# Kernel tuning notes

Measured on AMD Instinct MI355X. Metric: run time of the kernel, lower is better.

## Reference

```python
import jax, jax.numpy as jnp
import numpy as np

DIM = 1024
HEADS = 16
DIM_HEAD = 64
INNER = HEADS * DIM_HEAD
SCALE = DIM_HEAD ** -0.5


def setup_inputs() -> dict:
    key = jax.random.key(0)
    k1, k2, k3 = jax.random.split(key, 3)
    b, n = 2, 2048
    x = jax.random.normal(k1, (b, n, DIM), dtype=jnp.float32)
    mask = jnp.ones((b, n), dtype=bool)
    # to_qkv: Linear(dim, 3*inner, bias=False) stored as [dim, 3*inner]
    w_qkv = jax.random.normal(k2, (DIM, 3 * INNER), dtype=jnp.float32) * (DIM ** -0.5)
    # to_out: Linear(inner, dim, bias=False) stored as [inner, dim]
    w_out = jax.random.normal(k3, (INNER, DIM), dtype=jnp.float32) * (INNER ** -0.5)
    g = jnp.ones((DIM,), dtype=jnp.float32)  # LayerNorm gain
    return {"x": x, "mask": mask, "w_qkv": w_qkv, "w_out": w_out, "g": g}


def _layernorm(x, g):
    eps = 1e-5 if x.dtype == jnp.float32 else 1e-3
    mean = jnp.mean(x, axis=-1, keepdims=True)
    var = jnp.var(x, axis=-1, keepdims=True)  # unbiased=False
    return (x - mean) * jax.lax.rsqrt(var + eps) * g


def reference(x, mask, w_qkv, w_out, g):
    b, n, _ = x.shape
    qkv = x @ w_qkv  # [b, n, 3*inner]
    q, k, v = jnp.split(qkv, 3, axis=-1)
    # b n (h d) -> b h n d
    split_heads = lambda t: t.reshape(b, n, HEADS, DIM_HEAD).transpose(0, 2, 1, 3)
    q, k, v = split_heads(q), split_heads(k), split_heads(v)
    q = q * SCALE
    sim = jnp.einsum('bhid,bhjd->bhij', q, k)  # [b, h, n, n]
    mask_value = -jnp.finfo(sim.dtype).max
    key_mask = mask[:, None, None, :]  # b 1 1 j
    sim = jnp.where(key_mask, sim, mask_value)
    causal_mask = jnp.triu(jnp.ones((n, n), dtype=bool), k=1)
    sim = jnp.where(causal_mask, mask_value, sim)
    attn = jax.nn.softmax(sim.astype(jnp.float32), axis=-1).astype(sim.dtype)
    out = jnp.einsum('bhij,bhjd->bhid', attn, v)
    out = out.transpose(0, 2, 1, 3).reshape(b, n, INNER)  # b h n d -> b n (h d)
    out = out @ w_out
    return _layernorm(out, g)
```

## Files before the change

### kernel.cpp

```cpp
#include <hip/hip_runtime.h>
#include <hip/hip_bf16.h>


typedef __bf16 bf16_t;
typedef __bf16 bf16x8 __attribute__((ext_vector_type(8)));
typedef __bf16 bf16x4 __attribute__((ext_vector_type(4)));
typedef float  f32x4  __attribute__((ext_vector_type(4)));
typedef short  s16x4  __attribute__((ext_vector_type(4)));

#define DIMX   1024
#define HEADS  16
#define DHEAD  64
#define INNER  1024
#define SEQ    2048
#define BATCH  2
#define NROWS  (BATCH * SEQ)
#define QKV_N  (3 * INNER)
#define NQT    (SEQ / 64)
#define QK2SCALE 0.18033688011f

__device__ __forceinline__ bf16_t f2b(float f) { return (bf16_t)f; }

__device__ __forceinline__ void gload16(const bf16_t* g, bf16_t* s) {
  __builtin_amdgcn_global_load_lds(
      (const __attribute__((address_space(1))) unsigned int*)g,
      (__attribute__((address_space(3))) unsigned int*)s, 16, 0, 0);
}

__device__ __forceinline__ f32x4 mfma16(bf16x8 a, bf16x8 b, f32x4 c) {
  return __builtin_amdgcn_mfma_f32_16x16x32_bf16(a, b, c, 0, 0, 0);
}

__device__ __forceinline__ f32x4 pv_mfma(bf16x4 a, bf16x4 b, f32x4 c) {
  s16x4 as, bs;
  __builtin_memcpy(&as, &a, 8);
  __builtin_memcpy(&bs, &b, 8);
#if __has_builtin(__builtin_amdgcn_mfma_f32_16x16x16bf16_1k)
  return __builtin_amdgcn_mfma_f32_16x16x16bf16_1k(as, bs, c, 0, 0, 0);
#else
  f32x4 d = c;
  asm("v_mfma_f32_16x16x16_bf16 %0, %1, %2, %0" : "+v"(d) : "v"(as), "v"(bs));
  return d;
#endif
}

__global__ __launch_bounds__(256)
void prep_all(const float* __restrict__ x, const float* __restrict__ w_qkv,
              const float* __restrict__ w_out, bf16_t* __restrict__ xb,
              bf16_t* __restrict__ wqkvT, bf16_t* __restrict__ woutT) {
  __shared__ float tile[32][33];
  const int bid = blockIdx.x;
  if (bid < 4096) {
    const int i = bid * 256 + threadIdx.x;
    float4 v = *(const float4*)&x[(size_t)i * 4];
    bf16x4 o;
    o[0] = f2b(v.x); o[1] = f2b(v.y); o[2] = f2b(v.z); o[3] = f2b(v.w);
    *(bf16x4*)&xb[(size_t)i * 4] = o;
    return;
  }
  const float* in; bf16_t* out; int R, C, bx, by;
  if (bid < 4096 + 3072) {
    const int t1 = bid - 4096;
    in = w_qkv; out = wqkvT; R = DIMX; C = QKV_N; bx = t1 % 96; by = t1 / 96;
  } else {
    const int t2 = bid - 7168;
    in = w_out; out = woutT; R = DIMX; C = DIMX; bx = t2 & 31; by = t2 >> 5;
  }
  const int c0 = bx * 32, r0 = by * 32;
  const int tx = threadIdx.x & 31, ty = threadIdx.x >> 5;
  #pragma unroll
  for (int i = 0; i < 32; i += 8)
    tile[ty + i][tx] = in[(size_t)(r0 + ty + i) * C + c0 + tx];
  __syncthreads();
  #pragma unroll
  for (int i = 0; i < 32; i += 8)
    out[(size_t)(c0 + ty + i) * R + r0 + tx] = f2b(tile[tx][ty + i]);
}

__global__ __launch_bounds__(256)
void vtrans(const bf16_t* __restrict__ qkv, bf16_t* __restrict__ vt) {
  __shared__ bf16_t t[64][66];
  const int bh = blockIdx.y;
  const int b = bh >> 4, h = bh & 15;
  const int j0 = blockIdx.x * 64;
  const int tx = threadIdx.x & 63, ty = threadIdx.x >> 6;
  #pragma unroll
  for (int i = 0; i < 64; i += 4)
    t[ty + i][tx] = qkv[(size_t)(b * SEQ + j0 + ty + i) * QKV_N + 2 * INNER + h * 64 + tx];
  __syncthreads();
  #pragma unroll
  for (int i = 0; i < 64; i += 4)
    vt[((size_t)bh * 64 + ty + i) * SEQ + j0 + tx] = t[tx][ty + i];
}

template<int OUT_F32>
__global__ __launch_bounds__(256)
void gemm_bt(const bf16_t* __restrict__ A, const bf16_t* __restrict__ Bt,
             void* __restrict__ Cp, int M, int N, int K) {
  constexpr int BK = 64;
  __shared__ bf16_t As[128 * BK];
  __shared__ bf16_t Bs[128 * BK];
  const int t = threadIdx.x;
  const int w = t >> 6, l = t & 63, lo = l & 15, hi = l >> 4;
  const int nwg = gridDim.x * gridDim.y;
  int flat = blockIdx.y * gridDim.x + blockIdx.x;
  if ((nwg & 7) == 0) flat = (flat & 7) * (nwg >> 3) + (flat >> 3);
  const int m0 = (flat / gridDim.x) * 128, n0 = (flat % gridDim.x) * 128;
  const int wm = (w >> 1) * 64, wn = (w & 1) * 64;
  const int sl  = l >> 3;
  const int sgc = ((l & 7) ^ sl) * 8;
  const int r7  = lo & 7;
  f32x4 acc[4][4] = {};
  for (int k0 = 0; k0 < K; k0 += BK) {
    #pragma unroll
    for (int c = 0; c < 4; ++c) {
      const int rb = w * 32 + c * 8;
      gload16(&A [(size_t)(m0 + rb + sl) * K + k0 + sgc], &As[rb * BK + l * 8]);
      gload16(&Bt[(size_t)(n0 + rb + sl) * K + k0 + sgc], &Bs[rb * BK + l * 8]);
    }
    __syncthreads();
    #pragma unroll
    for (int kk = 0; kk < 2; ++kk) {
      bf16x8 af[4], bfr[4];
      #pragma unroll
      for (int mi = 0; mi < 4; ++mi)
        af[mi] = *(const bf16x8*)&As[(wm + mi * 16 + lo) * BK +
                                     (((kk * 4 + hi) ^ r7) << 3)];
      #pragma unroll
      for (int nj = 0; nj < 4; ++nj)
        bfr[nj] = *(const bf16x8*)&Bs[(wn + nj * 16 + lo) * BK +
                                      (((kk * 4 + hi) ^ r7) << 3)];
      __builtin_amdgcn_s_setprio(1);
      #pragma unroll
      for (int mi = 0; mi < 4; ++mi)
        #pragma unroll
        for (int nj = 0; nj < 4; ++nj)
          acc[mi][nj] = mfma16(af[mi], bfr[nj], acc[mi][nj]);
      __builtin_amdgcn_s_setprio(0);
    }
    __syncthreads();
  }
  #pragma unroll
  for (int mi = 0; mi < 4; ++mi)
    #pragma unroll
    for (int nj = 0; nj < 4; ++nj)
      #pragma unroll
      for (int r = 0; r < 4; ++r) {
        size_t row = m0 + wm + mi * 16 + hi * 4 + r;
        size_t col = n0 + wn + nj * 16 + lo;
        if (OUT_F32)
          ((float*)Cp)[row * N + col] = acc[mi][nj][r];
        else
          ((bf16_t*)Cp)[row * N + col] = f2b(acc[mi][nj][r]);
      }
}

__global__ __launch_bounds__(256, 4)
void attn_fa10(const bf16_t* __restrict__ qkv, const bf16_t* __restrict__ vt,
               bf16_t* __restrict__ attn_out, bf16_t* __restrict__ pacc,
               float* __restrict__ plsum) {
  const int bx  = blockIdx.x;
  const int xcd = bx & 7, idx = bx >> 3;
  const int bh  = xcd * 4 + (idx & 3);
  const int ta  = (idx >> 2) & 15;
  const int half = idx >> 6;
  const int tb  = NQT - 1 - ta;
  const int b = bh >> 4, h = bh & 15;
  const int t = threadIdx.x, w = t >> 6, l = t & 63, lo = l & 15, hi = l >> 4;

  __shared__ bf16_t Ks[2][64 * 64];
  __shared__ bf16_t Vs[2][64 * 64];

  const int srow = l >> 3;
  const int sgc  = ((l & 7) ^ srow) * 8;
  const size_t kgbase = (size_t)(b * SEQ) * QKV_N + INNER + h * 64;
  const size_t vgbase = (size_t)bh * 64 * SEQ;

  auto STAGE = [&](int ti, int buf) {
    const int j0 = ti * 64;
    #pragma unroll
    for (int c = 0; c < 2; ++c) {
      const int rb = w * 16 + c * 8;
      gload16(&qkv[kgbase + (size_t)(j0 + rb + srow) * QKV_N + sgc],
              &Ks[buf][rb * 64]);
      gload16(&vt[vgbase + (size_t)(rb + srow) * SEQ + j0 + sgc],
              &Vs[buf][rb * 64]);
    }
  };

  const int r7 = lo & 7;
  bf16x4 vone4;
  #pragma unroll
  for (int i = 0; i < 4; ++i) vone4[i] = f2b(1.0f);
  f32x4 acc[4];
  f32x4 acc_l;

  auto SEG = [&](const int qt, const int t0, const int t1, const bool dmask) {
    const size_t qb = (size_t)(b * SEQ + qt * 64 + w * 16 + lo) * QKV_N + h * 64;
    bf16x8 qf0 = *(const bf16x8*)&qkv[qb + hi * 8];
    bf16x8 qf1 = *(const bf16x8*)&qkv[qb + 32 + hi * 8];
    #pragma unroll
    for (int i = 0; i < 8; ++i) {
      qf0[i] = f2b((float)qf0[i] * QK2SCALE);
      qf1[i] = f2b((float)qf1[i] * QK2SCALE);
    }
    f32x4 z4 = {};
    acc[0] = z4; acc[1] = z4; acc[2] = z4; acc[3] = z4;
    acc_l = z4;

    STAGE(t0, 0);
    __syncthreads();
    for (int ti = t0; ti <= t1; ++ti) {
      const int buf = (ti - t0) & 1;
      if (ti + 1 <= t1) STAGE(ti + 1, buf ^ 1);
      const bool mB = dmask && (ti == t1);
      const int jcap = mB ? w : 3;
      __builtin_amdgcn_s_setprio(1);
      #pragma unroll
      for (int jb = 0; jb < 4; ++jb) {
        if (jb <= jcap) {
          const bf16_t* kp = &Ks[buf][(jb * 16 + lo) * 64];
          bf16x8 kf0 = *(const bf16x8*)&kp[(hi ^ r7) << 3];
          bf16x8 kf1 = *(const bf16x8*)&kp[((hi + 4) ^ r7) << 3];
          f32x4 z = {};
          z = mfma16(kf0, qf0, z);
          z = mfma16(kf1, qf1, z);
          const bool dm = mB && (jb == w);
          bf16x4 p;
          #pragma unroll
          for (int r = 0; r < 4; ++r) {
            float pe = exp2f(z[r]);
            if (dm && (hi * 4 + r > lo)) pe = 0.f;
            p[r] = f2b(pe);
          }
          #pragma unroll
          for (int dj = 0; dj < 4; ++dj) {
            bf16x4 vf = *(const bf16x4*)&Vs[buf][(dj * 16 + lo) * 64 +
                        (((2 * jb + (hi >> 1)) ^ r7) << 3) + ((hi & 1) << 2)];
            acc[dj] = pv_mfma(p, vf, acc[dj]);
          }
          acc_l = pv_mfma(p, vone4, acc_l);
        }
      }
      __builtin_amdgcn_s_setprio(0);
      __syncthreads();
    }
  };

  if (half == 0) {
    SEG(ta, 0, ta, true);
    #pragma unroll
    for (int r = 0; r < 4; ++r) {
      const float lr = 1.f / acc_l[r];
      #pragma unroll
      for (int dj = 0; dj < 4; ++dj)
        attn_out[(size_t)(b * SEQ + ta * 64 + w * 16 + hi * 4 + r) * INNER +
                 h * 64 + dj * 16 + lo] = f2b(acc[dj][r] * lr);
    }
    SEG(tb, 0, 15 - ta, false);
    {
      const int prb = (bh * 16 + (tb - 16)) * 64;
      #pragma unroll
      for (int dj = 0; dj < 4; ++dj)
        #pragma unroll
        for (int r = 0; r < 4; ++r)
          pacc[(size_t)(prb + w * 16 + hi * 4 + r) * 64 + dj * 16 + lo] =
              f2b(acc[dj][r]);
      if (lo == 0) {
        #pragma unroll
        for (int r = 0; r < 4; ++r)
          plsum[prb + w * 16 + hi * 4 + r] = acc_l[r];
      }
    }
  } else {
    SEG(tb, 16 - ta, tb, true);
    {
      const int prb = (bh * 16 + (tb - 16)) * 64;
      #pragma unroll
      for (int dj = 0; dj < 4; ++dj)
        #pragma unroll
        for (int r = 0; r < 4; ++r)
          pacc[2097152 + (size_t)(prb + w * 16 + hi * 4 + r) * 64 + dj * 16 + lo] =
              f2b(acc[dj][r]);
      if (lo == 0) {
        #pragma unroll
        for (int r = 0; r < 4; ++r)
          plsum[32768 + prb + w * 16 + hi * 4 + r] = acc_l[r];
      }
    }
  }
}

__global__ __launch_bounds__(256)
void attn_combine(const bf16_t* __restrict__ pacc, const float* __restrict__ plsum,
                  bf16_t* __restrict__ attn_out) {
  const int g = blockIdx.x * 256 + threadIdx.x;
  const int d8 = g & 7;
  const int row = g >> 3;
  const int qr = row & 63, qt = 16 + ((row >> 6) & 15), bh = row >> 10;
  const int b = bh >> 4, h = bh & 15;
  bf16x8 xa = *(const bf16x8*)&pacc[(size_t)row * 64 + d8 * 8];
  bf16x8 ya = *(const bf16x8*)&pacc[2097152 + (size_t)row * 64 + d8 * 8];
  const float inv = 1.f / (plsum[row] + plsum[32768 + row]);
  bf16x8 o;
  #pragma unroll
  for (int i = 0; i < 8; ++i)
    o[i] = f2b(((float)xa[i] + (float)ya[i]) * inv);
  *(bf16x8*)&attn_out[(size_t)(b * SEQ + qt * 64 + qr) * INNER + h * 64 + d8 * 8] = o;
}

__global__ __launch_bounds__(256)
void layernorm_b(const bf16_t* __restrict__ in, const float* __restrict__ g,
                 float* __restrict__ out) {
  const int row = blockIdx.x;
  const bf16_t* xr = in + (size_t)row * DIMX;
  const int c = threadIdx.x * 4;
  bf16x4 v4 = *(const bf16x4*)&xr[c];
  const float vx = (float)v4[0], vy = (float)v4[1], vz = (float)v4[2], vw = (float)v4[3];
  float s = vx + vy + vz + vw;
  float q = vx * vx + vy * vy + vz * vz + vw * vw;
  #pragma unroll
  for (int o = 32; o > 0; o >>= 1) {
    s += __shfl_down(s, o);
    q += __shfl_down(q, o);
  }
  __shared__ float rs[4], rq[4];
  const int wid = threadIdx.x >> 6;
  if ((threadIdx.x & 63) == 0) { rs[wid] = s; rq[wid] = q; }
  __syncthreads();
  s = rs[0] + rs[1] + rs[2] + rs[3];
  q = rq[0] + rq[1] + rq[2] + rq[3];
  const float mean = s * (1.f / DIMX);
  const float var  = q * (1.f / DIMX) - mean * mean;
  const float inv  = rsqrtf(var + 1e-5f);
  float4 gv = *(const float4*)&g[c];
  float4 o4;
  o4.x = (vx - mean) * inv * gv.x;
  o4.y = (vy - mean) * inv * gv.y;
  o4.z = (vz - mean) * inv * gv.z;
  o4.w = (vw - mean) * inv * gv.w;
  *(float4*)&out[(size_t)row * DIMX + c] = o4;
}

extern "C" void kernel_launch(void* const* d_in, const int* in_sizes, int n_in,
                              void* d_out, int out_size, void* d_ws, size_t ws_size,
                              hipStream_t stream) {
  const float* x     = (const float*)d_in[0];
  const float* w_qkv = (const float*)d_in[2];
  const float* w_out = (const float*)d_in[3];
  const float* g     = (const float*)d_in[4];

  char* ws = (char*)d_ws;
  const size_t MB = 1024 * 1024;
  bf16_t* xb     = (bf16_t*)(ws);
  bf16_t* wqkvT  = (bf16_t*)(ws + 8 * MB);
  bf16_t* woutT  = (bf16_t*)(ws + 14 * MB);
  bf16_t* qkv    = (bf16_t*)(ws + 16 * MB);
  bf16_t* vt     = (bf16_t*)(ws + 40 * MB);
  bf16_t* attn_o = (bf16_t*)(ws + 48 * MB);
  bf16_t* pacc   = (bf16_t*)(ws);
  float*  plsum  = (float*) (ws + 8 * MB);
  bf16_t* outpre = (bf16_t*)(ws + 16 * MB);

  prep_all<<<8192, 256, 0, stream>>>(x, w_qkv, w_out, xb, wqkvT, woutT);

  gemm_bt<0><<<dim3(QKV_N / 128, NROWS / 128), 256, 0, stream>>>(
      xb, wqkvT, qkv, NROWS, QKV_N, DIMX);

  vtrans<<<dim3(SEQ / 64, BATCH * HEADS), 256, 0, stream>>>(qkv, vt);

  attn_fa10<<<dim3(1024), 256, 0, stream>>>(qkv, vt, attn_o, pacc, plsum);
  attn_combine<<<dim3(1024), 256, 0, stream>>>(pacc, plsum, attn_o);

  gemm_bt<0><<<dim3(DIMX / 128, NROWS / 128), 256, 0, stream>>>(
      attn_o, woutT, outpre, NROWS, DIMX, DIMX);

  layernorm_b<<<NROWS, 256, 0, stream>>>(outpre, g, (float*)d_out);
}
```

Before: 118.2 us.

## Pair key blocks into 16x16x32 MFMAs for PV and use native exp2

The attention inner loop now processes two 16-key blocks at a time, packing their probabilities into an 8-wide bf16 fragment so the PV product and the row-sum use the 16x16x32 MFMA instead of two 16x16x16 MFMAs. This halves the number of PV/rowsum MFMA issues. exp2 switches to the hardware builtin, and the causal mask is now computed from global indices. The barrier moves to the top of each iteration. The cost is extra register shuffling to assemble V fragments from two 4-wide LDS reads, plus some wasted exp work on masked blocks.

```diff
diff --git a/kernel.cpp b/kernel.cpp
--- a/kernel.cpp
+++ b/kernel.cpp
@@ -6,7 +6,6 @@
 typedef __bf16 bf16x8 __attribute__((ext_vector_type(8)));
 typedef __bf16 bf16x4 __attribute__((ext_vector_type(4)));
 typedef float  f32x4  __attribute__((ext_vector_type(4)));
-typedef short  s16x4  __attribute__((ext_vector_type(4)));
 
 #define DIMX   1024
 #define HEADS  16
@@ -21,6 +20,14 @@
 
 __device__ __forceinline__ bf16_t f2b(float f) { return (bf16_t)f; }
 
+__device__ __forceinline__ float fexp2(float x) {
+#if __has_builtin(__builtin_amdgcn_exp2f)
+  return __builtin_amdgcn_exp2f(x);
+#else
+  return exp2f(x);
+#endif
+}
+
 __device__ __forceinline__ void gload16(const bf16_t* g, bf16_t* s) {
   __builtin_amdgcn_global_load_lds(
       (const __attribute__((address_space(1))) unsigned int*)g,
@@ -29,19 +36,6 @@
 
 __device__ __forceinline__ f32x4 mfma16(bf16x8 a, bf16x8 b, f32x4 c) {
   return __builtin_amdgcn_mfma_f32_16x16x32_bf16(a, b, c, 0, 0, 0);
-}
-
-__device__ __forceinline__ f32x4 pv_mfma(bf16x4 a, bf16x4 b, f32x4 c) {
-  s16x4 as, bs;
-  __builtin_memcpy(&as, &a, 8);
-  __builtin_memcpy(&bs, &b, 8);
-#if __has_builtin(__builtin_amdgcn_mfma_f32_16x16x16bf16_1k)
-  return __builtin_amdgcn_mfma_f32_16x16x16bf16_1k(as, bs, c, 0, 0, 0);
-#else
-  f32x4 d = c;
-  asm("v_mfma_f32_16x16x16_bf16 %0, %1, %2, %0" : "+v"(d) : "v"(as), "v"(bs));
-  return d;
-#endif
 }
 
 __global__ __launch_bounds__(256)
@@ -156,7 +150,7 @@
 }
 
 __global__ __launch_bounds__(256, 4)
-void attn_fa10(const bf16_t* __restrict__ qkv, const bf16_t* __restrict__ vt,
+void attn_fa12(const bf16_t* __restrict__ qkv, const bf16_t* __restrict__ vt,
                bf16_t* __restrict__ attn_out, bf16_t* __restrict__ pacc,
                float* __restrict__ plsum) {
   const int bx  = blockIdx.x;
@@ -189,9 +183,9 @@
   };
 
   const int r7 = lo & 7;
-  bf16x4 vone4;
-  #pragma unroll
-  for (int i = 0; i < 4; ++i) vone4[i] = f2b(1.0f);
+  bf16x8 vone8;
+  #pragma unroll
+  for (int i = 0; i < 8; ++i) vone8[i] = f2b(1.0f);
   f32x4 acc[4];
   f32x4 acc_l;
 
@@ -204,47 +198,62 @@
       qf0[i] = f2b((float)qf0[i] * QK2SCALE);
       qf1[i] = f2b((float)qf1[i] * QK2SCALE);
     }
-    f32x4 z4 = {};
-    acc[0] = z4; acc[1] = z4; acc[2] = z4; acc[3] = z4;
-    acc_l = z4;
+    const f32x4 fz = {};
+    acc[0] = fz; acc[1] = fz; acc[2] = fz; acc[3] = fz;
+    acc_l = fz;
+    const int qrow = qt * 64 + w * 16 + lo;
 
     STAGE(t0, 0);
-    __syncthreads();
     for (int ti = t0; ti <= t1; ++ti) {
       const int buf = (ti - t0) & 1;
+      __syncthreads();
       if (ti + 1 <= t1) STAGE(ti + 1, buf ^ 1);
       const bool mB = dmask && (ti == t1);
-      const int jcap = mB ? w : 3;
       __builtin_amdgcn_s_setprio(1);
       #pragma unroll
-      for (int jb = 0; jb < 4; ++jb) {
-        if (jb <= jcap) {
-          const bf16_t* kp = &Ks[buf][(jb * 16 + lo) * 64];
-          bf16x8 kf0 = *(const bf16x8*)&kp[(hi ^ r7) << 3];
-          bf16x8 kf1 = *(const bf16x8*)&kp[((hi + 4) ^ r7) << 3];
-          f32x4 z = {};
-          z = mfma16(kf0, qf0, z);
-          z = mfma16(kf1, qf1, z);
-          const bool dm = mB && (jb == w);
-          bf16x4 p;
+      for (int pr = 0; pr < 2; ++pr) {
+        const int jb0 = pr * 2;
+        if (!(mB && jb0 > w)) {
+          bf16x8 pa;
           #pragma unroll
-          for (int r = 0; r < 4; ++r) {
-            float pe = exp2f(z[r]);
-            if (dm && (hi * 4 + r > lo)) pe = 0.f;
-            p[r] = f2b(pe);
+          for (int q = 0; q < 2; ++q) {
+            const int jb = jb0 + q;
+            f32x4 z = fz;
+            if (!(mB && jb > w)) {
+              const bf16_t* kp = &Ks[buf][(jb * 16 + lo) * 64];
+              bf16x8 kf0 = *(const bf16x8*)&kp[(hi ^ r7) << 3];
+              bf16x8 kf1 = *(const bf16x8*)&kp[((hi + 4) ^ r7) << 3];
+              z = mfma16(kf0, qf0, z);
+              z = mfma16(kf1, qf1, z);
+            }
+            #pragma unroll
+            for (int r = 0; r < 4; ++r) {
+              float pe = fexp2(z[r]);
+              if (mB) {
+                const int jglob = ti * 64 + jb * 16 + hi * 4 + r;
+                if (jglob > qrow) pe = 0.f;
+              }
+              pa[q * 4 + r] = f2b(pe);
+            }
           }
           #pragma unroll
           for (int dj = 0; dj < 4; ++dj) {
-            bf16x4 vf = *(const bf16x4*)&Vs[buf][(dj * 16 + lo) * 64 +
-                        (((2 * jb + (hi >> 1)) ^ r7) << 3) + ((hi & 1) << 2)];
-            acc[dj] = pv_mfma(p, vf, acc[dj]);
+            const bf16_t* vp = &Vs[buf][(dj * 16 + lo) * 64];
+            bf16x4 va = *(const bf16x4*)&vp[
+                (((2 * jb0 + (hi >> 1)) ^ r7) << 3) + ((hi & 1) << 2)];
+            bf16x4 vb = *(const bf16x4*)&vp[
+                (((2 * jb0 + 2 + (hi >> 1)) ^ r7) << 3) + ((hi & 1) << 2)];
+            bf16x8 vf;
+            #pragma unroll
+            for (int i = 0; i < 4; ++i) { vf[i] = va[i]; vf[i + 4] = vb[i]; }
+            acc[dj] = mfma16(pa, vf, acc[dj]);
           }
-          acc_l = pv_mfma(p, vone4, acc_l);
+          acc_l = mfma16(pa, vone8, acc_l);
         }
       }
       __builtin_amdgcn_s_setprio(0);
-      __syncthreads();
-    }
+    }
+    __syncthreads();
   };
 
   if (half == 0) {
@@ -369,7 +378,7 @@
 
   vtrans<<<dim3(SEQ / 64, BATCH * HEADS), 256, 0, stream>>>(qkv, vt);
 
-  attn_fa10<<<dim3(1024), 256, 0, stream>>>(qkv, vt, attn_o, pacc, plsum);
+  attn_fa12<<<dim3(1024), 256, 0, stream>>>(qkv, vt, attn_o, pacc, plsum);
   attn_combine<<<dim3(1024), 256, 0, stream>>>(pacc, plsum, attn_o);
 
   gemm_bt<0><<<dim3(DIMX / 128, NROWS / 128), 256, 0, stream>>>(
```

Result: faster. 112.4 us (-4.9%).
